# Kernel tuning notes

Measured on AMD Instinct MI355X. Metric: run time of the kernel, lower is better.

Reference implementation:

```python
import jax, jax.numpy as jnp
import numpy as np

B, T, C = 1, 2048, 1024
H, HKV, DH, WIN = 16, 4, 64, 128
EPS = 1e-5


def rotate_half(x):
    x1, x2 = jnp.split(x, 2, axis=-1)
    return jnp.concatenate((-x2, x1), axis=-1)


def setup_inputs() -> dict:
    key = jax.random.key(0)
    ks = jax.random.split(key, 8)
    s = 0.02
    return {
        "x": jax.random.normal(ks[0], (B, T, C), dtype=jnp.float32),
        "Wq": jax.random.normal(ks[1], (C, H * DH), dtype=jnp.float32) * s,
        "Wk": jax.random.normal(ks[2], (C, HKV * DH), dtype=jnp.float32) * s,
        "Wv": jax.random.normal(ks[3], (C, HKV * DH), dtype=jnp.float32) * s,
        "Wc": jax.random.normal(ks[4], (C, C), dtype=jnp.float32) * s,
        "Wg": jax.random.normal(ks[5], (C, H), dtype=jnp.float32) * s,
        "bg": jax.random.normal(ks[6], (H,), dtype=jnp.float32) * s,
        "rms_w": jnp.ones((C,), dtype=jnp.float32),
    }


def reference(x, Wq, Wk, Wv, Wc, Wg, bg, rms_w):
    n_rep = H // HKV
    # projections -> [B, heads, T, DH]
    q = (x @ Wq).reshape(B, T, H, DH).transpose(0, 2, 1, 3)
    k = (x @ Wk).reshape(B, T, HKV, DH).transpose(0, 2, 1, 3)
    v = (x @ Wv).reshape(B, T, HKV, DH).transpose(0, 2, 1, 3)
    # rotary embedding (freqs duplicated across the two halves)
    inv_freq = 1.0 / (10000.0 ** (jnp.arange(0, DH, 2, dtype=jnp.float32) / DH))
    freqs = jnp.arange(T, dtype=jnp.float32)[:, None] * inv_freq[None, :]
    emb = jnp.concatenate((freqs, freqs), axis=-1)  # [T, DH]
    cos, sin = jnp.cos(emb)[None, None], jnp.sin(emb)[None, None]
    q = q * cos + rotate_half(q) * sin
    k = k * cos + rotate_half(k) * sin
    # GQA: repeat kv heads (contiguous repeat matches torch expand+reshape)
    k = jnp.repeat(k, n_rep, axis=1)
    v = jnp.repeat(v, n_rep, axis=1)
    # gated decay
    gate_logits = (x @ Wg + bg).reshape(B, T, H, 1).transpose(0, 2, 1, 3)  # [B,H,T,1]
    log_alpha = jax.nn.log_sigmoid(gate_logits)
    log_in_scale = jax.nn.log_sigmoid(-gate_logits)
    k_scaled = k * jnp.exp(log_in_scale)
    la_cum = jnp.cumsum(log_alpha, axis=2)                  # [B,H,T,1]
    log_decay = la_cum - jnp.swapaxes(la_cum, 2, 3)         # [B,H,T,T]
    causal = jnp.triu(jnp.ones((T, T), dtype=bool), k=1)
    decay = jnp.exp(jnp.where(causal, -jnp.inf, log_decay))
    scores = jnp.einsum('bhtd,bhsd->bhts', q, k_scaled)
    y_global = jnp.einsum('bhts,bhsd->bhtd', scores * decay, v)
    nb = T // WIN
    qb = q.reshape(B, H, nb, WIN, DH)
    kb = k.reshape(B, H, nb, WIN, DH)
    vb = v.reshape(B, H, nb, WIN, DH)
    att = jnp.einsum('bhnqd,bhnkd->bhnqk', qb, kb) / jnp.sqrt(jnp.float32(DH))
    wmask = jnp.triu(jnp.ones((WIN, WIN), dtype=bool), k=1)
    att = jax.nn.softmax(jnp.where(wmask, -jnp.inf, att), axis=-1)
    y_local = jnp.einsum('bhnqk,bhnkd->bhnqd', att, vb).reshape(B, H, T, DH)
    # fuse, RMSNorm, output projection
    y = (y_global + y_local).transpose(0, 2, 1, 3).reshape(B, T, C)
    y = y * jax.lax.rsqrt(jnp.mean(y * y, axis=-1, keepdims=True) + EPS) * rms_w
    return y @ Wc
```

## Files before the change

kernel.cpp:

```cpp
#include <hip/hip_runtime.h>
#include <hip/hip_bf16.h>


typedef __attribute__((ext_vector_type(8))) short bf16x8;
typedef __attribute__((ext_vector_type(4))) float f32x4;

#define MFMA16(a, b, c) __builtin_amdgcn_mfma_f32_16x16x32_bf16(a, b, c, 0, 0, 0)
#define LN10000_OVER_32 0.28782313662425575f

__device__ __forceinline__ short f2b(float f) {
  __hip_bfloat16 h = __float2bfloat16(f);
  return *reinterpret_cast<short*>(&h);
}
__device__ __forceinline__ float b2f(short s) {
  return __uint_as_float(((unsigned)(unsigned short)s) << 16);
}
__device__ __forceinline__ void gload16(const void* g, void* l) {
  __builtin_amdgcn_global_load_lds(
      (const __attribute__((address_space(1))) void*)g,
      (__attribute__((address_space(3))) void*)l, 16, 0, 0);
}

__device__ __forceinline__ void transpose_cvt_body(
    const float* __restrict__ src, short* __restrict__ dst, int R, int C,
    int bx, int by, float* ts ) {
  int c0 = bx * 32, r0 = by * 32;
  int tr = threadIdx.x >> 3, tc = (threadIdx.x & 7) * 4;
  float4 v = *(const float4*)&src[(size_t)(r0 + tr) * C + c0 + tc];
  ts[tr * 33 + tc] = v.x;
  ts[tr * 33 + tc + 1] = v.y;
  ts[tr * 33 + tc + 2] = v.z;
  ts[tr * 33 + tc + 3] = v.w;
  __syncthreads();
  alignas(8) short o[4];
#pragma unroll
  for (int i = 0; i < 4; ++i) o[i] = f2b(ts[(tc + i) * 33 + tr]);
  *(uint2*)&dst[(size_t)(c0 + tr) * R + r0 + tc] = *(uint2*)o;
}

__global__ __launch_bounds__(256) void prep_fused(
    const float* __restrict__ x, const float* __restrict__ Wq,
    const float* __restrict__ Wk, const float* __restrict__ Wv,
    const float* __restrict__ Wc, const float* __restrict__ Wg,
    const float* __restrict__ bg, short* __restrict__ xb,
    short* __restrict__ wqkvT, short* __restrict__ wcT,
    float* __restrict__ g) {
  __shared__ float ts[32 * 33];
  const int j = blockIdx.x;
  const int tid = threadIdx.x;
  if (j < 2048) {
    const int t = j;
    const int h = tid & 15, chunk = tid >> 4;
    const float* xr = x + (size_t)t * 1024 + chunk * 64;
    const float* wg = Wg + (size_t)chunk * 64 * 16 + h;
    float acc = 0.f;
#pragma unroll
    for (int c = 0; c < 64; c += 4) {
      float4 xv = *(const float4*)(xr + c);
      acc = fmaf(xv.x, wg[(c + 0) * 16], acc);
      acc = fmaf(xv.y, wg[(c + 1) * 16], acc);
      acc = fmaf(xv.z, wg[(c + 2) * 16], acc);
      acc = fmaf(xv.w, wg[(c + 3) * 16], acc);
    }
    ts[chunk * 16 + h] = acc;
    __syncthreads();
    if (tid < 16) {
      float s = bg[tid];
#pragma unroll
      for (int i = 0; i < 16; ++i) s += ts[i * 16 + tid];
      g[t * 16 + tid] = s;
    }
  } else if (j < 3072) {
    int i = ((j - 2048) * 256 + tid) * 8;
    float4 a = *(const float4*)(x + i);
    float4 b = *(const float4*)(x + i + 4);
    alignas(16) short o[8] = {f2b(a.x), f2b(a.y), f2b(a.z), f2b(a.w),
                              f2b(b.x), f2b(b.y), f2b(b.z), f2b(b.w)};
    *(float4*)(xb + i) = *(float4*)o;
  } else if (j < 4096) {
    int jj = j - 3072;
    transpose_cvt_body(Wq, wqkvT, 1024, 1024, jj & 31, jj >> 5, ts);
  } else if (j < 4352) {
    int jj = j - 4096;
    transpose_cvt_body(Wk, wqkvT + 1024 * 1024, 1024, 256, jj & 7, jj >> 3, ts);
  } else if (j < 4608) {
    int jj = j - 4352;
    transpose_cvt_body(Wv, wqkvT + 1280 * 1024, 1024, 256, jj & 7, jj >> 3, ts);
  } else {
    int jj = j - 4608;
    transpose_cvt_body(Wc, wcT, 1024, 1024, jj & 31, jj >> 5, ts);
  }
}

__global__ __launch_bounds__(256) void qkv_gemm_fused(
    const short* __restrict__ A, const short* __restrict__ Bt,
    short* __restrict__ qkvb, short* __restrict__ vtb,
    short* __restrict__ ktb, const float* __restrict__ g,
    float* __restrict__ lac, float* __restrict__ insc) {
  __shared__ short As[64 * 64];
  __shared__ short Bs[64 * 64];
  __shared__ float part[256];
  const int id = blockIdx.x;
  const int tid = threadIdx.x;
  if (id >= 768) {
    const int h = id - 768;
    float vals[8];
    float local = 0.f;
#pragma unroll
    for (int i = 0; i < 8; ++i) {
      int t = tid * 8 + i;
      float gv = g[t * 16 + h];
      float la = (gv > 0.f) ? -log1pf(expf(-gv)) : (gv - log1pf(expf(gv)));
      insc[h * 2048 + t] = 1.f / (1.f + expf(gv));
      vals[i] = la;
      local += la;
    }
    part[tid] = local;
    __syncthreads();
    for (int off = 1; off < 256; off <<= 1) {
      float add = (tid >= off) ? part[tid - off] : 0.f;
      __syncthreads();
      part[tid] += add;
      __syncthreads();
    }
    float run = (tid > 0) ? part[tid - 1] : 0.f;
#pragma unroll
    for (int i = 0; i < 8; ++i) {
      run += vals[i];
      lac[h * 2048 + tid * 8 + i] = run;
    }
    return;
  }
  const int lane = tid & 63, wid = tid >> 6;
  const int l15 = lane & 15, lq = lane >> 4;
  const int jlin = id >> 3;
  const int by = (id & 7) + 8 * (jlin / 24);
  const int bx = jlin % 24;
  const int m0 = by * 64, n0 = bx * 64;
  const int K = 1024;
  const int srow = lane >> 3;
  const int sc16 = (lane & 7) ^ srow;
  f32x4 acc[4];
#pragma unroll
  for (int nt = 0; nt < 4; ++nt) acc[nt] = {0.f, 0.f, 0.f, 0.f};
  for (int kt = 0; kt < K; kt += 64) {
    __syncthreads();
#pragma unroll
    for (int i = 0; i < 2; ++i) {
      int jj = wid * 2 + i;
      int row = jj * 8 + srow;
      gload16(A + (size_t)(m0 + row) * K + kt + sc16 * 8, &As[jj * 512]);
      gload16(Bt + (size_t)(n0 + row) * K + kt + sc16 * 8, &Bs[jj * 512]);
    }
    __syncthreads();
    bf16x8 af[2], bfr[4][2];
#pragma unroll
    for (int ks = 0; ks < 2; ++ks) {
      int c16 = ks * 4 + lq;
      int ar = wid * 16 + l15;
      af[ks] = *(const bf16x8*)&As[(ar * 8 + (c16 ^ (ar & 7))) * 8];
#pragma unroll
      for (int nt = 0; nt < 4; ++nt) {
        int br = nt * 16 + l15;
        bfr[nt][ks] = *(const bf16x8*)&Bs[(br * 8 + (c16 ^ (br & 7))) * 8];
      }
    }
#pragma unroll
    for (int ks = 0; ks < 2; ++ks)
#pragma unroll
      for (int nt = 0; nt < 4; ++nt)
        acc[nt] = MFMA16(af[ks], bfr[nt][ks], acc[nt]);
  }
  const int row0 = m0 + wid * 16 + lq * 4;
  if (bx >= 20) {
#pragma unroll
    for (int nt = 0; nt < 4; ++nt) {
      int vcol = (n0 - 1280) + nt * 16 + l15;
      alignas(8) short o4[4];
#pragma unroll
      for (int r = 0; r < 4; ++r) o4[r] = f2b(acc[nt][r]);
      *(uint2*)&vtb[(size_t)vcol * 2048 + row0] = *(uint2*)o4;
    }
    return;
  }
  const bool isk = (bx >= 16);
#pragma unroll
  for (int nt = 0; nt < 2; ++nt) {
    int d = nt * 16 + l15;
    float ivf = __expf(-LN10000_OVER_32 * (float)d);
    alignas(8) short oa[4], ob[4];
#pragma unroll
    for (int r = 0; r < 4; ++r) {
      int row_g = row0 + r;
      float th = (float)row_g * ivf;
      float cs = cosf(th), sn = sinf(th);
      float a = acc[nt][r], b = acc[nt + 2][r];
      oa[r] = f2b(a * cs - b * sn);
      ob[r] = f2b(b * cs + a * sn);
      qkvb[(size_t)row_g * 1536 + n0 + d] = oa[r];
      qkvb[(size_t)row_g * 1536 + n0 + d + 32] = ob[r];
    }
    if (isk) {
      int dk = n0 - 1024 + d;
      *(uint2*)&ktb[(size_t)dk * 2048 + row0] = *(uint2*)oa;
      *(uint2*)&ktb[(size_t)(dk + 32) * 2048 + row0] = *(uint2*)ob;
    }
  }
}

__global__ __launch_bounds__(256) void p1_local(
    const short* __restrict__ qkv, const short* __restrict__ vtb,
    const short* __restrict__ ktb, const float* __restrict__ lac,
    const float* __restrict__ insc, float* __restrict__ Bmat,
    short* __restrict__ yl) {
  __shared__ short SA[64 * 64];
  __shared__ short SB[128 * 64];
  __shared__ short SC[64 * 128];
  __shared__ short SD[64 * 128];
  __shared__ float lacs[64], inss[64], gvals[64];
  const int tid = threadIdx.x, lane = tid & 63, wid = tid >> 6;
  const int l15 = lane & 15, lq = lane >> 4;
  const int h = blockIdx.y;
  const int kh = h >> 2;
  if (blockIdx.z == 0) {
    const int c = blockIdx.x;
    short* Ks = SB;
    short* Vts = SC;
    const int srow = lane >> 3;
    const int sc16 = (lane & 7) ^ srow;
#pragma unroll
    for (int i = 0; i < 2; ++i) {
      int jj = wid * 2 + i;
      int row = jj * 8 + srow;
      gload16(ktb + (size_t)(kh * 64 + row) * 2048 + c * 64 + sc16 * 8,
              &Ks[jj * 512]);
      gload16(vtb + (size_t)(kh * 64 + row) * 2048 + c * 64 + sc16 * 8,
              &Vts[jj * 512]);
    }
    if (tid < 64) {
      lacs[tid] = lac[h * 2048 + c * 64 + tid];
      inss[tid] = insc[h * 2048 + c * 64 + tid];
    }
    __syncthreads();
    if (tid < 64)
      gvals[tid] = __expf(fminf(lacs[63] - lacs[tid], 0.f)) * inss[tid];
    __syncthreads();
    const int er = wid * 16 + l15;
    bf16x8 av[2];
#pragma unroll
    for (int ks = 0; ks < 2; ++ks) {
      int c16 = ks * 4 + lq;
      bf16x8 raw = *(const bf16x8*)&Vts[(er * 8 + (c16 ^ (er & 7))) * 8];
      float4 g0 = *(const float4*)&gvals[c16 * 8];
      float4 g1 = *(const float4*)&gvals[c16 * 8 + 4];
      float gv[8] = {g0.x, g0.y, g0.z, g0.w, g1.x, g1.y, g1.z, g1.w};
      bf16x8 sc;
#pragma unroll
      for (int jx = 0; jx < 8; ++jx) sc[jx] = f2b(b2f(raw[jx]) * gv[jx]);
      av[ks] = sc;
    }
    f32x4 acc[4];
#pragma unroll
    for (int nt = 0; nt < 4; ++nt) acc[nt] = {0.f, 0.f, 0.f, 0.f};
#pragma unroll
    for (int ks = 0; ks < 2; ++ks) {
      int c16 = ks * 4 + lq;
#pragma unroll
      for (int nt = 0; nt < 4; ++nt) {
        int dr = nt * 16 + l15;
        bf16x8 bk = *(const bf16x8*)&Ks[(dr * 8 + (c16 ^ (dr & 7))) * 8];
        acc[nt] = MFMA16(av[ks], bk, acc[nt]);
      }
    }
    float* Bout = Bmat + (size_t)(h * 32 + c) * 4096;
#pragma unroll
    for (int nt = 0; nt < 4; ++nt)
#pragma unroll
      for (int r = 0; r < 4; ++r) {
        int e = wid * 16 + lq * 4 + r;
        Bout[e * 64 + nt * 16 + l15] = acc[nt][r];
      }
  } else {
    const int half = blockIdx.x & 1, wb = blockIdx.x >> 1;
    const int t0 = wb * 128;
    short* Qs = SA;
    short* Ks = SB;
    short* Vts = SC;
    short* Ps = SD;
#pragma unroll
    for (int i = 0; i < 2; ++i) {
      int cix = tid + 256 * i;
      int row = cix >> 3, cc = cix & 7;
      *(float4*)&Qs[(row * 8 + (cc ^ (row & 7))) * 8] =
          *(const float4*)&qkv[(size_t)(t0 + half * 64 + row) * 1536 + h * 64 + cc * 8];
    }
#pragma unroll
    for (int i = 0; i < 4; ++i) {
      int cix = tid + 256 * i;
      int row = cix >> 3, cc = cix & 7;
      *(float4*)&Ks[(row * 8 + (cc ^ (row & 7))) * 8] =
          *(const float4*)&qkv[(size_t)(t0 + row) * 1536 + 1024 + kh * 64 + cc * 8];
    }
#pragma unroll
    for (int i = 0; i < 4; ++i) {
      int cix = tid + 256 * i;
      int row = cix >> 4, cc = cix & 15;
      int sw = (row * 16 + ((cc & 8) | ((cc & 7) ^ (row & 7)))) * 8;
      *(float4*)&Vts[sw] =
          *(const float4*)&vtb[(size_t)(kh * 64 + row) * 2048 + t0 + cc * 8];
    }
    __syncthreads();
    const int qr = wid * 16 + l15;
    bf16x8 aq[2];
#pragma unroll
    for (int ks = 0; ks < 2; ++ks) {
      int c16 = ks * 4 + lq;
      aq[ks] = *(const bf16x8*)&Qs[(qr * 8 + (c16 ^ (qr & 7))) * 8];
    }
    f32x4 sv[2][4];
    const int nst = half + 1;
    for (int st = 0; st < nst; ++st)
#pragma unroll
      for (int nt = 0; nt < 4; ++nt) {
        int kr = st * 64 + nt * 16 + l15;
        bf16x8 bk0 = *(const bf16x8*)&Ks[(kr * 8 + ((0 + lq) ^ (kr & 7))) * 8];
        bf16x8 bk1 = *(const bf16x8*)&Ks[(kr * 8 + ((4 + lq) ^ (kr & 7))) * 8];
        f32x4 z = {0.f, 0.f, 0.f, 0.f};
        z = MFMA16(aq[0], bk0, z);
        z = MFMA16(aq[1], bk1, z);
        sv[st][nt] = z;
      }
    float mrow[4], ssum[4];
#pragma unroll
    for (int r = 0; r < 4; ++r) mrow[r] = -1e30f;
    for (int st = 0; st < nst; ++st)
#pragma unroll
      for (int nt = 0; nt < 4; ++nt) {
        int col = st * 64 + nt * 16 + l15;
#pragma unroll
        for (int r = 0; r < 4; ++r) {
          int row = half * 64 + wid * 16 + lq * 4 + r;
          float v = (col <= row) ? sv[st][nt][r] * 0.125f : -1e30f;
          sv[st][nt][r] = v;
          mrow[r] = fmaxf(mrow[r], v);
        }
      }
#pragma unroll
    for (int r = 0; r < 4; ++r) {
      for (int off = 1; off < 16; off <<= 1)
        mrow[r] = fmaxf(mrow[r], __shfl_xor(mrow[r], off, 64));
      ssum[r] = 0.f;
    }
    for (int st = 0; st < nst; ++st)
#pragma unroll
      for (int nt = 0; nt < 4; ++nt) {
        int col = st * 64 + nt * 16 + l15;
#pragma unroll
        for (int r = 0; r < 4; ++r) {
          float e = __expf(sv[st][nt][r] - mrow[r]);
          ssum[r] += e;
          int row = wid * 16 + lq * 4 + r;
          int c16 = col >> 3;
          Ps[(row * 16 + ((c16 & 8) | ((c16 & 7) ^ (row & 7)))) * 8 + (col & 7)] =
              f2b(e);
        }
      }
#pragma unroll
    for (int r = 0; r < 4; ++r) {
      for (int off = 1; off < 16; off <<= 1) ssum[r] += __shfl_xor(ssum[r], off, 64);
      ssum[r] = 1.f / ssum[r];
    }
    __syncthreads();
    f32x4 o[4];
#pragma unroll
    for (int nt = 0; nt < 4; ++nt) o[nt] = {0.f, 0.f, 0.f, 0.f};
    for (int ks = 0; ks < nst * 2; ++ks) {
      int c16 = ks * 4 + lq;
      bf16x8 ap = *(const bf16x8*)&Ps[(qr * 16 + ((c16 & 8) | ((c16 & 7) ^ (qr & 7)))) * 8];
#pragma unroll
      for (int nt = 0; nt < 4; ++nt) {
        int vr = nt * 16 + l15;
        bf16x8 bv = *(const bf16x8*)&Vts[(vr * 16 + ((c16 & 8) | ((c16 & 7) ^ (vr & 7)))) * 8];
        o[nt] = MFMA16(ap, bv, o[nt]);
      }
    }
#pragma unroll
    for (int nt = 0; nt < 4; ++nt)
#pragma unroll
      for (int r = 0; r < 4; ++r) {
        int row_g = t0 + half * 64 + wid * 16 + lq * 4 + r;
        int colg = h * 64 + nt * 16 + l15;
        yl[(size_t)row_g * 1024 + colg] = f2b(o[nt][r] * ssum[r]);
      }
  }
}

__global__ __launch_bounds__(256) void scan_kernel(
    const float* __restrict__ Bmat, const float* __restrict__ lac,
    short* __restrict__ St) {
  const int h = blockIdx.x, tid = threadIdx.x;
  __shared__ float lacE[32];
  if (tid < 32) lacE[tid] = lac[h * 2048 + tid * 64 + 63];
  __syncthreads();
  const int base = tid * 16;
  float S[16];
#pragma unroll
  for (int i = 0; i < 16; ++i) S[i] = 0.f;
  alignas(16) short z16[16];
#pragma unroll
  for (int i = 0; i < 16; ++i) z16[i] = 0;
  *(uint4*)&St[(size_t)(h * 32) * 4096 + base] = *(uint4*)z16;
  *(uint4*)&St[(size_t)(h * 32) * 4096 + base + 8] = *(uint4*)(z16 + 8);
  for (int c = 1; c < 32; ++c) {
    float a = (c >= 2) ? __expf(fminf(lacE[c - 1] - lacE[c - 2], 0.f)) : 0.f;
    const float* Bp = Bmat + (size_t)(h * 32 + c - 1) * 4096 + base;
    float4 b0 = *(const float4*)(Bp + 0);
    float4 b1 = *(const float4*)(Bp + 4);
    float4 b2 = *(const float4*)(Bp + 8);
    float4 b3 = *(const float4*)(Bp + 12);
    float bb[16] = {b0.x, b0.y, b0.z, b0.w, b1.x, b1.y, b1.z, b1.w,
                    b2.x, b2.y, b2.z, b2.w, b3.x, b3.y, b3.z, b3.w};
    alignas(16) short o16[16];
#pragma unroll
    for (int i = 0; i < 16; ++i) {
      S[i] = fmaf(a, S[i], bb[i]);
      o16[i] = f2b(S[i]);
    }
    *(uint4*)&St[(size_t)(h * 32 + c) * 4096 + base] = *(uint4*)o16;
    *(uint4*)&St[(size_t)(h * 32 + c) * 4096 + base + 8] = *(uint4*)(o16 + 8);
  }
}

__global__ __launch_bounds__(256) void global_attn_v3(
    const short* __restrict__ qkv, const short* __restrict__ vtb,
    const short* __restrict__ St, const float* __restrict__ lac,
    const float* __restrict__ insc, short* __restrict__ yg) {
  const int c = blockIdx.x, h = blockIdx.y;
  const int kh = h >> 2;
  __shared__ short Qs[64 * 64], Ks[64 * 64], Vts[64 * 64], Sts[64 * 64],
      Ps[64 * 64];
  __shared__ float lacq[64], inss[64];
  __shared__ float laprev_sh;
  const int tid = threadIdx.x, lane = tid & 63, wid = tid >> 6;
  const int l15 = lane & 15, lq = lane >> 4;
  const int srow = lane >> 3;
  const int sc16 = (lane & 7) ^ srow;
#pragma unroll
  for (int i = 0; i < 2; ++i) {
    int jj = wid * 2 + i;
    int row = jj * 8 + srow;
    gload16(qkv + (size_t)(c * 64 + row) * 1536 + h * 64 + sc16 * 8,
            &Qs[jj * 512]);
    gload16(qkv + (size_t)(c * 64 + row) * 1536 + 1024 + kh * 64 + sc16 * 8,
            &Ks[jj * 512]);
    gload16(vtb + (size_t)(kh * 64 + row) * 2048 + c * 64 + sc16 * 8,
            &Vts[jj * 512]);
    gload16(St + (size_t)(h * 32 + c) * 4096 + row * 64 + sc16 * 8,
            &Sts[jj * 512]);
  }
  if (tid < 64) {
    lacq[tid] = lac[h * 2048 + c * 64 + tid];
    inss[tid] = insc[h * 2048 + c * 64 + tid];
  }
  if (tid == 0) laprev_sh = (c > 0) ? lac[h * 2048 + c * 64 - 1] : 1e30f;
  __syncthreads();
  const int qr = wid * 16 + l15;
  bf16x8 aq[2];
#pragma unroll
  for (int ks = 0; ks < 2; ++ks) {
    int c16 = ks * 4 + lq;
    aq[ks] = *(const bf16x8*)&Qs[(qr * 8 + (c16 ^ (qr & 7))) * 8];
  }
  f32x4 sv[4];
#pragma unroll
  for (int nt = 0; nt < 4; ++nt) {
    int kr = nt * 16 + l15;
    bf16x8 bk0 = *(const bf16x8*)&Ks[(kr * 8 + ((0 + lq) ^ (kr & 7))) * 8];
    bf16x8 bk1 = *(const bf16x8*)&Ks[(kr * 8 + ((4 + lq) ^ (kr & 7))) * 8];
    f32x4 z = {0.f, 0.f, 0.f, 0.f};
    z = MFMA16(aq[0], bk0, z);
    z = MFMA16(aq[1], bk1, z);
    sv[nt] = z;
  }
#pragma unroll
  for (int nt = 0; nt < 4; ++nt) {
    int col = nt * 16 + l15;
    float ls = lacq[col], is = inss[col];
#pragma unroll
    for (int r = 0; r < 4; ++r) {
      int row = wid * 16 + lq * 4 + r;
      float d = lacq[row] - ls;
      float w = __expf(fminf(d, 0.f)) * is;
      if (col > row) w = 0.f;
      Ps[(row * 8 + ((col >> 3) ^ (row & 7))) * 8 + (col & 7)] = f2b(sv[nt][r] * w);
    }
  }
  f32x4 oi[4];
#pragma unroll
  for (int nt = 0; nt < 4; ++nt) {
    int er = nt * 16 + l15;
    bf16x8 bs0 = *(const bf16x8*)&Sts[(er * 8 + ((0 + lq) ^ (er & 7))) * 8];
    bf16x8 bs1 = *(const bf16x8*)&Sts[(er * 8 + ((4 + lq) ^ (er & 7))) * 8];
    f32x4 z = {0.f, 0.f, 0.f, 0.f};
    z = MFMA16(aq[0], bs0, z);
    z = MFMA16(aq[1], bs1, z);
    oi[nt] = z;
  }
  __syncthreads();
  bf16x8 ap[2];
#pragma unroll
  for (int ks = 0; ks < 2; ++ks) {
    int c16 = ks * 4 + lq;
    ap[ks] = *(const bf16x8*)&Ps[(qr * 8 + (c16 ^ (qr & 7))) * 8];
  }
  f32x4 o[4];
#pragma unroll
  for (int nt = 0; nt < 4; ++nt) {
    int vr = nt * 16 + l15;
    bf16x8 bv0 = *(const bf16x8*)&Vts[(vr * 8 + ((0 + lq) ^ (vr & 7))) * 8];
    bf16x8 bv1 = *(const bf16x8*)&Vts[(vr * 8 + ((4 + lq) ^ (vr & 7))) * 8];
    f32x4 z = {0.f, 0.f, 0.f, 0.f};
    z = MFMA16(ap[0], bv0, z);
    z = MFMA16(ap[1], bv1, z);
    o[nt] = z;
  }
  const float laprev = laprev_sh;
#pragma unroll
  for (int r = 0; r < 4; ++r) {
    int row = wid * 16 + lq * 4 + r;
    float rfac = __expf(fminf(lacq[row] - laprev, 0.f));
    int row_g = c * 64 + row;
#pragma unroll
    for (int nt = 0; nt < 4; ++nt) {
      int colg = h * 64 + nt * 16 + l15;
      yg[(size_t)row_g * 1024 + colg] = f2b(o[nt][r] + rfac * oi[nt][r]);
    }
  }
}

__global__ __launch_bounds__(256) void rmsnorm_fuse(
    const short* __restrict__ yg, const short* __restrict__ ylc,
    const float* __restrict__ w, short* __restrict__ yn) {
  const int t = blockIdx.x, tid = threadIdx.x;
  __shared__ float red[4];
  __shared__ float rowv[1024];
  __shared__ float scale_sh;
  float ssum = 0.f;
  for (int c = tid; c < 1024; c += 256) {
    size_t idx = (size_t)t * 1024 + c;
    float v = b2f(yg[idx]) + b2f(ylc[idx]);
    rowv[c] = v;
    ssum = fmaf(v, v, ssum);
  }
  for (int off = 32; off > 0; off >>= 1) ssum += __shfl_down(ssum, off, 64);
  const int lane = tid & 63, wd = tid >> 6;
  if (lane == 0) red[wd] = ssum;
  __syncthreads();
  if (tid == 0)
    scale_sh = rsqrtf((red[0] + red[1] + red[2] + red[3]) * (1.0f / 1024.0f) + 1e-5f);
  __syncthreads();
  const float scale = scale_sh;
  for (int c = tid; c < 1024; c += 256)
    yn[(size_t)t * 1024 + c] = f2b(rowv[c] * scale * w[c]);
}

__global__ __launch_bounds__(256) void out_gemm(
    const short* __restrict__ A, const short* __restrict__ Bt,
    float* __restrict__ C, int M, int N, int K, int nbx) {
  __shared__ short As[64 * 64];
  __shared__ short Bs[64 * 64];
  const int tid = threadIdx.x, lane = tid & 63, wid = tid >> 6;
  const int l15 = lane & 15, lq = lane >> 4;
  const int id = blockIdx.x;
  const int jlin = id >> 3;
  const int by = (id & 7) + 8 * (jlin / nbx);
  const int bx = jlin % nbx;
  const int m0 = by * 64, n0 = bx * 64;
  const int srow = lane >> 3;
  const int sc16 = (lane & 7) ^ srow;
  f32x4 acc[4];
#pragma unroll
  for (int nt = 0; nt < 4; ++nt) acc[nt] = {0.f, 0.f, 0.f, 0.f};
  for (int kt = 0; kt < K; kt += 64) {
    __syncthreads();
#pragma unroll
    for (int i = 0; i < 2; ++i) {
      int jj = wid * 2 + i;
      int row = jj * 8 + srow;
      gload16(A + (size_t)(m0 + row) * K + kt + sc16 * 8, &As[jj * 512]);
      gload16(Bt + (size_t)(n0 + row) * K + kt + sc16 * 8, &Bs[jj * 512]);
    }
    __syncthreads();
    bf16x8 af[2], bfr[4][2];
#pragma unroll
    for (int ks = 0; ks < 2; ++ks) {
      int c16 = ks * 4 + lq;
      int ar = wid * 16 + l15;
      af[ks] = *(const bf16x8*)&As[(ar * 8 + (c16 ^ (ar & 7))) * 8];
#pragma unroll
      for (int nt = 0; nt < 4; ++nt) {
        int br = nt * 16 + l15;
        bfr[nt][ks] = *(const bf16x8*)&Bs[(br * 8 + (c16 ^ (br & 7))) * 8];
      }
    }
#pragma unroll
    for (int ks = 0; ks < 2; ++ks)
#pragma unroll
      for (int nt = 0; nt < 4; ++nt)
        acc[nt] = MFMA16(af[ks], bfr[nt][ks], acc[nt]);
  }
#pragma unroll
  for (int r = 0; r < 4; ++r) {
    int row_g = m0 + wid * 16 + lq * 4 + r;
#pragma unroll
    for (int nt = 0; nt < 4; ++nt)
      C[(size_t)row_g * N + n0 + nt * 16 + l15] = acc[nt][r];
  }
}

extern "C" void kernel_launch(void* const* d_in, const int* in_sizes, int n_in,
                              void* d_out, int out_size, void* d_ws,
                              size_t ws_size, hipStream_t stream) {
  const float* x = (const float*)d_in[0];
  const float* Wq = (const float*)d_in[1];
  const float* Wk = (const float*)d_in[2];
  const float* Wv = (const float*)d_in[3];
  const float* Wc = (const float*)d_in[4];
  const float* Wg = (const float*)d_in[5];
  const float* bg = (const float*)d_in[6];
  const float* rmsw = (const float*)d_in[7];
  float* out = (float*)d_out;

  short* wqkvT = (short*)d_ws;
  short* wcT = wqkvT + 1536 * 1024;
  short* qkvb = wcT + 1024 * 1024;
  short* vtb = qkvb + 2048 * 1536;
  short* ktb = vtb + 256 * 2048;
  float* gw = (float*)(ktb + 256 * 2048);
  float* lacw = gw + 2048 * 16;
  float* inscw = lacw + 16 * 2048;
  float* Bmat = inscw + 16 * 2048;
  short* Stb = (short*)(Bmat + 16 * 32 * 4096);
  short* xb = Stb + 16 * 32 * 4096;
  short* yg = xb;
  short* ylc = xb + 2048 * 1024;
  short* yn = ylc + 2048 * 1024;

  prep_fused<<<5632, 256, 0, stream>>>(x, Wq, Wk, Wv, Wc, Wg, bg, xb, wqkvT,
                                       wcT, gw);
  qkv_gemm_fused<<<784, 256, 0, stream>>>(xb, wqkvT, qkvb, vtb, ktb, gw, lacw,
                                          inscw);
  p1_local<<<dim3(32, 16, 2), 256, 0, stream>>>(qkvb, vtb, ktb, lacw, inscw,
                                                Bmat, ylc);
  scan_kernel<<<16, 256, 0, stream>>>(Bmat, lacw, Stb);
  global_attn_v3<<<dim3(32, 16), 256, 0, stream>>>(qkvb, vtb, Stb, lacw, inscw,
                                                   yg);
  rmsnorm_fuse<<<2048, 256, 0, stream>>>(yg, ylc, rmsw, yn);
  out_gemm<<<512, 256, 0, stream>>>(yn, wcT, out, 2048, 1024, 1024, 16);
}
```

Measured before the change: 149.7 us.

## Fuse RMSNorm into attention epilogue and output GEMM, retile QKV GEMM, prefetch scan

Removes the standalone RMSNorm kernel. The global attention epilogue now adds the local output, writes the unnormalized sum and atomically accumulates per-row sum of squares. rms_w is folded into the transposed Wc, and the output GEMM applies the rsqrt scale per row. The QKV GEMM moves to 128-row tiles, halving the block count, the output GEMM uses a 2x2 warp layout, and the scan kernel prefetches the next chunk's Bmat. This saves a kernel launch and a round trip of the activations through memory, but adds atomics and a zeroing step, and the larger QKV tile lowers the number of blocks.

New measurement: 150.8 us. No clear change (+0.7%).

```diff
diff --git a/kernel.cpp b/kernel.cpp
--- a/kernel.cpp
+++ b/kernel.cpp
@@ -23,7 +23,7 @@
 
 __device__ __forceinline__ void transpose_cvt_body(
     const float* __restrict__ src, short* __restrict__ dst, int R, int C,
-    int bx, int by, float* ts ) {
+    int bx, int by, float* ts , const float* __restrict__ sw) {
   int c0 = bx * 32, r0 = by * 32;
   int tr = threadIdx.x >> 3, tc = (threadIdx.x & 7) * 4;
   float4 v = *(const float4*)&src[(size_t)(r0 + tr) * C + c0 + tc];
@@ -34,7 +34,10 @@
   __syncthreads();
   alignas(8) short o[4];
 #pragma unroll
-  for (int i = 0; i < 4; ++i) o[i] = f2b(ts[(tc + i) * 33 + tr]);
+  for (int i = 0; i < 4; ++i) {
+    float m = sw ? sw[r0 + tc + i] : 1.0f;
+    o[i] = f2b(ts[(tc + i) * 33 + tr] * m);
+  }
   *(uint2*)&dst[(size_t)(c0 + tr) * R + r0 + tc] = *(uint2*)o;
 }
 
@@ -42,9 +45,9 @@
     const float* __restrict__ x, const float* __restrict__ Wq,
     const float* __restrict__ Wk, const float* __restrict__ Wv,
     const float* __restrict__ Wc, const float* __restrict__ Wg,
-    const float* __restrict__ bg, short* __restrict__ xb,
-    short* __restrict__ wqkvT, short* __restrict__ wcT,
-    float* __restrict__ g) {
+    const float* __restrict__ bg, const float* __restrict__ rmsw,
+    short* __restrict__ xb, short* __restrict__ wqkvT,
+    short* __restrict__ wcT, float* __restrict__ g, float* __restrict__ rs) {
   __shared__ float ts[32 * 33];
   const int j = blockIdx.x;
   const int tid = threadIdx.x;
@@ -79,16 +82,22 @@
     *(float4*)(xb + i) = *(float4*)o;
   } else if (j < 4096) {
     int jj = j - 3072;
-    transpose_cvt_body(Wq, wqkvT, 1024, 1024, jj & 31, jj >> 5, ts);
+    transpose_cvt_body(Wq, wqkvT, 1024, 1024, jj & 31, jj >> 5, ts, nullptr);
   } else if (j < 4352) {
     int jj = j - 4096;
-    transpose_cvt_body(Wk, wqkvT + 1024 * 1024, 1024, 256, jj & 7, jj >> 3, ts);
+    transpose_cvt_body(Wk, wqkvT + 1024 * 1024, 1024, 256, jj & 7, jj >> 3, ts,
+                       nullptr);
   } else if (j < 4608) {
     int jj = j - 4352;
-    transpose_cvt_body(Wv, wqkvT + 1280 * 1024, 1024, 256, jj & 7, jj >> 3, ts);
+    transpose_cvt_body(Wv, wqkvT + 1280 * 1024, 1024, 256, jj & 7, jj >> 3, ts,
+                       nullptr);
+  } else if (j < 5632) {
+    int jj = j - 4608;
+    transpose_cvt_body(Wc, wcT, 1024, 1024, jj & 31, jj >> 5, ts, rmsw);
   } else {
-    int jj = j - 4608;
-    transpose_cvt_body(Wc, wcT, 1024, 1024, jj & 31, jj >> 5, ts);
+    int i4 = ((j - 5632) * 256 + tid) * 4;
+    float4 z = {0.f, 0.f, 0.f, 0.f};
+    *(float4*)(rs + i4) = z;
   }
 }
 
@@ -97,13 +106,13 @@
     short* __restrict__ qkvb, short* __restrict__ vtb,
     short* __restrict__ ktb, const float* __restrict__ g,
     float* __restrict__ lac, float* __restrict__ insc) {
-  __shared__ short As[64 * 64];
+  __shared__ short As[128 * 64];
   __shared__ short Bs[64 * 64];
   __shared__ float part[256];
   const int id = blockIdx.x;
   const int tid = threadIdx.x;
-  if (id >= 768) {
-    const int h = id - 768;
+  if (id >= 384) {
+    const int h = id - 384;
     float vals[8];
     float local = 0.f;
 #pragma unroll
@@ -136,29 +145,39 @@
   const int jlin = id >> 3;
   const int by = (id & 7) + 8 * (jlin / 24);
   const int bx = jlin % 24;
-  const int m0 = by * 64, n0 = bx * 64;
+  const int m0 = by * 128, n0 = bx * 64;
   const int K = 1024;
   const int srow = lane >> 3;
   const int sc16 = (lane & 7) ^ srow;
-  f32x4 acc[4];
-#pragma unroll
-  for (int nt = 0; nt < 4; ++nt) acc[nt] = {0.f, 0.f, 0.f, 0.f};
+  f32x4 acc[2][4];
+#pragma unroll
+  for (int mt = 0; mt < 2; ++mt)
+#pragma unroll
+    for (int nt = 0; nt < 4; ++nt) acc[mt][nt] = {0.f, 0.f, 0.f, 0.f};
   for (int kt = 0; kt < K; kt += 64) {
     __syncthreads();
+#pragma unroll
+    for (int i = 0; i < 4; ++i) {
+      int jj = wid * 4 + i;
+      int row = jj * 8 + srow;
+      gload16(A + (size_t)(m0 + row) * K + kt + sc16 * 8, &As[jj * 512]);
+    }
 #pragma unroll
     for (int i = 0; i < 2; ++i) {
       int jj = wid * 2 + i;
       int row = jj * 8 + srow;
-      gload16(A + (size_t)(m0 + row) * K + kt + sc16 * 8, &As[jj * 512]);
       gload16(Bt + (size_t)(n0 + row) * K + kt + sc16 * 8, &Bs[jj * 512]);
     }
     __syncthreads();
-    bf16x8 af[2], bfr[4][2];
+    bf16x8 af[2][2], bfr[4][2];
 #pragma unroll
     for (int ks = 0; ks < 2; ++ks) {
       int c16 = ks * 4 + lq;
-      int ar = wid * 16 + l15;
-      af[ks] = *(const bf16x8*)&As[(ar * 8 + (c16 ^ (ar & 7))) * 8];
+#pragma unroll
+      for (int mt = 0; mt < 2; ++mt) {
+        int ar = wid * 32 + mt * 16 + l15;
+        af[mt][ks] = *(const bf16x8*)&As[(ar * 8 + (c16 ^ (ar & 7))) * 8];
+      }
 #pragma unroll
       for (int nt = 0; nt < 4; ++nt) {
         int br = nt * 16 + l15;
@@ -168,42 +187,51 @@
 #pragma unroll
     for (int ks = 0; ks < 2; ++ks)
 #pragma unroll
-      for (int nt = 0; nt < 4; ++nt)
-        acc[nt] = MFMA16(af[ks], bfr[nt][ks], acc[nt]);
-  }
-  const int row0 = m0 + wid * 16 + lq * 4;
+      for (int mt = 0; mt < 2; ++mt)
+#pragma unroll
+        for (int nt = 0; nt < 4; ++nt)
+          acc[mt][nt] = MFMA16(af[mt][ks], bfr[nt][ks], acc[mt][nt]);
+  }
   if (bx >= 20) {
 #pragma unroll
-    for (int nt = 0; nt < 4; ++nt) {
-      int vcol = (n0 - 1280) + nt * 16 + l15;
-      alignas(8) short o4[4];
-#pragma unroll
-      for (int r = 0; r < 4; ++r) o4[r] = f2b(acc[nt][r]);
-      *(uint2*)&vtb[(size_t)vcol * 2048 + row0] = *(uint2*)o4;
+    for (int mt = 0; mt < 2; ++mt) {
+      int row0 = m0 + wid * 32 + mt * 16 + lq * 4;
+#pragma unroll
+      for (int nt = 0; nt < 4; ++nt) {
+        int vcol = (n0 - 1280) + nt * 16 + l15;
+        alignas(8) short o4[4];
+#pragma unroll
+        for (int r = 0; r < 4; ++r) o4[r] = f2b(acc[mt][nt][r]);
+        *(uint2*)&vtb[(size_t)vcol * 2048 + row0] = *(uint2*)o4;
+      }
     }
     return;
   }
   const bool isk = (bx >= 16);
 #pragma unroll
-  for (int nt = 0; nt < 2; ++nt) {
-    int d = nt * 16 + l15;
-    float ivf = __expf(-LN10000_OVER_32 * (float)d);
-    alignas(8) short oa[4], ob[4];
-#pragma unroll
-    for (int r = 0; r < 4; ++r) {
-      int row_g = row0 + r;
-      float th = (float)row_g * ivf;
-      float cs = cosf(th), sn = sinf(th);
-      float a = acc[nt][r], b = acc[nt + 2][r];
-      oa[r] = f2b(a * cs - b * sn);
-      ob[r] = f2b(b * cs + a * sn);
-      qkvb[(size_t)row_g * 1536 + n0 + d] = oa[r];
-      qkvb[(size_t)row_g * 1536 + n0 + d + 32] = ob[r];
-    }
-    if (isk) {
-      int dk = n0 - 1024 + d;
-      *(uint2*)&ktb[(size_t)dk * 2048 + row0] = *(uint2*)oa;
-      *(uint2*)&ktb[(size_t)(dk + 32) * 2048 + row0] = *(uint2*)ob;
+  for (int mt = 0; mt < 2; ++mt) {
+    int row0 = m0 + wid * 32 + mt * 16 + lq * 4;
+#pragma unroll
+    for (int nt = 0; nt < 2; ++nt) {
+      int d = nt * 16 + l15;
+      float ivf = __expf(-LN10000_OVER_32 * (float)d);
+      alignas(8) short oa[4], ob[4];
+#pragma unroll
+      for (int r = 0; r < 4; ++r) {
+        int row_g = row0 + r;
+        float th = (float)row_g * ivf;
+        float cs = cosf(th), sn = sinf(th);
+        float a = acc[mt][nt][r], b = acc[mt][nt + 2][r];
+        oa[r] = f2b(a * cs - b * sn);
+        ob[r] = f2b(b * cs + a * sn);
+        qkvb[(size_t)row_g * 1536 + n0 + d] = oa[r];
+        qkvb[(size_t)row_g * 1536 + n0 + d + 32] = ob[r];
+      }
+      if (isk) {
+        int dk = n0 - 1024 + d;
+        *(uint2*)&ktb[(size_t)dk * 2048 + row0] = *(uint2*)oa;
+        *(uint2*)&ktb[(size_t)(dk + 32) * 2048 + row0] = *(uint2*)ob;
+      }
     }
   }
 }
@@ -411,15 +439,23 @@
   for (int i = 0; i < 16; ++i) z16[i] = 0;
   *(uint4*)&St[(size_t)(h * 32) * 4096 + base] = *(uint4*)z16;
   *(uint4*)&St[(size_t)(h * 32) * 4096 + base + 8] = *(uint4*)(z16 + 8);
+  const float* Bp0 = Bmat + (size_t)(h * 32) * 4096 + base;
+  float4 p0 = *(const float4*)(Bp0 + 0);
+  float4 p1 = *(const float4*)(Bp0 + 4);
+  float4 p2 = *(const float4*)(Bp0 + 8);
+  float4 p3 = *(const float4*)(Bp0 + 12);
   for (int c = 1; c < 32; ++c) {
+    float4 n0 = p0, n1 = p1, n2 = p2, n3 = p3;
+    if (c < 31) {
+      const float* Bn = Bmat + (size_t)(h * 32 + c) * 4096 + base;
+      n0 = *(const float4*)(Bn + 0);
+      n1 = *(const float4*)(Bn + 4);
+      n2 = *(const float4*)(Bn + 8);
+      n3 = *(const float4*)(Bn + 12);
+    }
     float a = (c >= 2) ? __expf(fminf(lacE[c - 1] - lacE[c - 2], 0.f)) : 0.f;
-    const float* Bp = Bmat + (size_t)(h * 32 + c - 1) * 4096 + base;
-    float4 b0 = *(const float4*)(Bp + 0);
-    float4 b1 = *(const float4*)(Bp + 4);
-    float4 b2 = *(const float4*)(Bp + 8);
-    float4 b3 = *(const float4*)(Bp + 12);
-    float bb[16] = {b0.x, b0.y, b0.z, b0.w, b1.x, b1.y, b1.z, b1.w,
-                    b2.x, b2.y, b2.z, b2.w, b3.x, b3.y, b3.z, b3.w};
+    float bb[16] = {p0.x, p0.y, p0.z, p0.w, p1.x, p1.y, p1.z, p1.w,
+                    p2.x, p2.y, p2.z, p2.w, p3.x, p3.y, p3.z, p3.w};
     alignas(16) short o16[16];
 #pragma unroll
     for (int i = 0; i < 16; ++i) {
@@ -428,13 +464,15 @@
     }
     *(uint4*)&St[(size_t)(h * 32 + c) * 4096 + base] = *(uint4*)o16;
     *(uint4*)&St[(size_t)(h * 32 + c) * 4096 + base + 8] = *(uint4*)(o16 + 8);
+    p0 = n0; p1 = n1; p2 = n2; p3 = n3;
   }
 }
 
 __global__ __launch_bounds__(256) void global_attn_v3(
     const short* __restrict__ qkv, const short* __restrict__ vtb,
     const short* __restrict__ St, const float* __restrict__ lac,
-    const float* __restrict__ insc, short* __restrict__ yg) {
+    const float* __restrict__ insc, const short* __restrict__ ylc,
+    short* __restrict__ ys, float* __restrict__ rs) {
   const int c = blockIdx.x, h = blockIdx.y;
   const int kh = h >> 2;
   __shared__ short Qs[64 * 64], Ks[64 * 64], Vts[64 * 64], Sts[64 * 64],
@@ -530,57 +568,41 @@
     int row = wid * 16 + lq * 4 + r;
     float rfac = __expf(fminf(lacq[row] - laprev, 0.f));
     int row_g = c * 64 + row;
+    float ssq = 0.f;
 #pragma unroll
     for (int nt = 0; nt < 4; ++nt) {
       int colg = h * 64 + nt * 16 + l15;
-      yg[(size_t)row_g * 1024 + colg] = f2b(o[nt][r] + rfac * oi[nt][r]);
-    }
-  }
-}
-
-__global__ __launch_bounds__(256) void rmsnorm_fuse(
-    const short* __restrict__ yg, const short* __restrict__ ylc,
-    const float* __restrict__ w, short* __restrict__ yn) {
-  const int t = blockIdx.x, tid = threadIdx.x;
-  __shared__ float red[4];
-  __shared__ float rowv[1024];
-  __shared__ float scale_sh;
-  float ssum = 0.f;
-  for (int c = tid; c < 1024; c += 256) {
-    size_t idx = (size_t)t * 1024 + c;
-    float v = b2f(yg[idx]) + b2f(ylc[idx]);
-    rowv[c] = v;
-    ssum = fmaf(v, v, ssum);
-  }
-  for (int off = 32; off > 0; off >>= 1) ssum += __shfl_down(ssum, off, 64);
-  const int lane = tid & 63, wd = tid >> 6;
-  if (lane == 0) red[wd] = ssum;
-  __syncthreads();
-  if (tid == 0)
-    scale_sh = rsqrtf((red[0] + red[1] + red[2] + red[3]) * (1.0f / 1024.0f) + 1e-5f);
-  __syncthreads();
-  const float scale = scale_sh;
-  for (int c = tid; c < 1024; c += 256)
-    yn[(size_t)t * 1024 + c] = f2b(rowv[c] * scale * w[c]);
+      size_t idx = (size_t)row_g * 1024 + colg;
+      float v = o[nt][r] + rfac * oi[nt][r] + b2f(ylc[idx]);
+      ys[idx] = f2b(v);
+      ssq = fmaf(v, v, ssq);
+    }
+    for (int off = 1; off < 16; off <<= 1) ssq += __shfl_xor(ssq, off, 64);
+    if (l15 == 0) atomicAdd(&rs[row_g], ssq);
+  }
 }
 
 __global__ __launch_bounds__(256) void out_gemm(
     const short* __restrict__ A, const short* __restrict__ Bt,
-    float* __restrict__ C, int M, int N, int K, int nbx) {
+    const float* __restrict__ rs, float* __restrict__ C) {
   __shared__ short As[64 * 64];
   __shared__ short Bs[64 * 64];
   const int tid = threadIdx.x, lane = tid & 63, wid = tid >> 6;
   const int l15 = lane & 15, lq = lane >> 4;
+  const int wm = wid >> 1, wn = wid & 1;
   const int id = blockIdx.x;
   const int jlin = id >> 3;
-  const int by = (id & 7) + 8 * (jlin / nbx);
-  const int bx = jlin % nbx;
+  const int by = (id & 7) + 8 * (jlin / 16);
+  const int bx = jlin % 16;
   const int m0 = by * 64, n0 = bx * 64;
+  const int K = 1024;
   const int srow = lane >> 3;
   const int sc16 = (lane & 7) ^ srow;
-  f32x4 acc[4];
-#pragma unroll
-  for (int nt = 0; nt < 4; ++nt) acc[nt] = {0.f, 0.f, 0.f, 0.f};
+  f32x4 acc[2][2];
+#pragma unroll
+  for (int mt = 0; mt < 2; ++mt)
+#pragma unroll
+    for (int nt = 0; nt < 2; ++nt) acc[mt][nt] = {0.f, 0.f, 0.f, 0.f};
   for (int kt = 0; kt < K; kt += 64) {
     __syncthreads();
 #pragma unroll
@@ -591,30 +613,41 @@
       gload16(Bt + (size_t)(n0 + row) * K + kt + sc16 * 8, &Bs[jj * 512]);
     }
     __syncthreads();
-    bf16x8 af[2], bfr[4][2];
+    bf16x8 af[2][2], bfr[2][2];
 #pragma unroll
     for (int ks = 0; ks < 2; ++ks) {
       int c16 = ks * 4 + lq;
-      int ar = wid * 16 + l15;
-      af[ks] = *(const bf16x8*)&As[(ar * 8 + (c16 ^ (ar & 7))) * 8];
-#pragma unroll
-      for (int nt = 0; nt < 4; ++nt) {
-        int br = nt * 16 + l15;
+#pragma unroll
+      for (int mt = 0; mt < 2; ++mt) {
+        int ar = wm * 32 + mt * 16 + l15;
+        af[mt][ks] = *(const bf16x8*)&As[(ar * 8 + (c16 ^ (ar & 7))) * 8];
+      }
+#pragma unroll
+      for (int nt = 0; nt < 2; ++nt) {
+        int br = wn * 32 + nt * 16 + l15;
         bfr[nt][ks] = *(const bf16x8*)&Bs[(br * 8 + (c16 ^ (br & 7))) * 8];
       }
     }
 #pragma unroll
     for (int ks = 0; ks < 2; ++ks)
 #pragma unroll
-      for (int nt = 0; nt < 4; ++nt)
-        acc[nt] = MFMA16(af[ks], bfr[nt][ks], acc[nt]);
-  }
-#pragma unroll
-  for (int r = 0; r < 4; ++r) {
-    int row_g = m0 + wid * 16 + lq * 4 + r;
-#pragma unroll
-    for (int nt = 0; nt < 4; ++nt)
-      C[(size_t)row_g * N + n0 + nt * 16 + l15] = acc[nt][r];
+      for (int mt = 0; mt < 2; ++mt)
+#pragma unroll
+        for (int nt = 0; nt < 2; ++nt)
+          acc[mt][nt] = MFMA16(af[mt][ks], bfr[nt][ks], acc[mt][nt]);
+  }
+#pragma unroll
+  for (int mt = 0; mt < 2; ++mt) {
+    int row0 = m0 + wm * 32 + mt * 16 + lq * 4;
+#pragma unroll
+    for (int r = 0; r < 4; ++r) {
+      int row_g = row0 + r;
+      float sc = rsqrtf(rs[row_g] * (1.0f / 1024.0f) + 1e-5f);
+#pragma unroll
+      for (int nt = 0; nt < 2; ++nt)
+        C[(size_t)row_g * 1024 + n0 + wn * 32 + nt * 16 + l15] =
+            acc[mt][nt][r] * sc;
+    }
   }
 }
 
@@ -642,19 +675,18 @@
   float* Bmat = inscw + 16 * 2048;
   short* Stb = (short*)(Bmat + 16 * 32 * 4096);
   short* xb = Stb + 16 * 32 * 4096;
-  short* yg = xb;
+  short* ys = xb;
   short* ylc = xb + 2048 * 1024;
-  short* yn = ylc + 2048 * 1024;
-
-  prep_fused<<<5632, 256, 0, stream>>>(x, Wq, Wk, Wv, Wc, Wg, bg, xb, wqkvT,
-                                       wcT, gw);
-  qkv_gemm_fused<<<784, 256, 0, stream>>>(xb, wqkvT, qkvb, vtb, ktb, gw, lacw,
+  float* rsq = (float*)(ylc + 2048 * 1024);
+
+  prep_fused<<<5634, 256, 0, stream>>>(x, Wq, Wk, Wv, Wc, Wg, bg, rmsw, xb,
+                                       wqkvT, wcT, gw, rsq);
+  qkv_gemm_fused<<<400, 256, 0, stream>>>(xb, wqkvT, qkvb, vtb, ktb, gw, lacw,
                                           inscw);
   p1_local<<<dim3(32, 16, 2), 256, 0, stream>>>(qkvb, vtb, ktb, lacw, inscw,
                                                 Bmat, ylc);
   scan_kernel<<<16, 256, 0, stream>>>(Bmat, lacw, Stb);
   global_attn_v3<<<dim3(32, 16), 256, 0, stream>>>(qkvb, vtb, Stb, lacw, inscw,
-                                                   yg);
-  rmsnorm_fuse<<<2048, 256, 0, stream>>>(yg, ylc, rmsw, yn);
-  out_gemm<<<512, 256, 0, stream>>>(yn, wcT, out, 2048, 1024, 1024, 16);
-}
+                                                   ylc, ys, rsq);
+  out_gemm<<<512, 256, 0, stream>>>(ys, wcT, rsq, out);
+}
```
